# Kernel optimization log

Hardware: AMD Instinct MI355X
Metric: run time of the kernel (lower is better)

Reference implementation:

```python
import jax, jax.numpy as jnp
import numpy as np


def setup_inputs() -> dict:
    key = jax.random.key(0)
    ks = jax.random.split(key, 8)
    C = 128
    Cq = C // 8  # 16
    x = jax.random.normal(ks[0], (4, C, 64, 64), dtype=jnp.float32)
    s = 1.0 / np.sqrt(C)
    wq = jax.random.normal(ks[1], (Cq, C), dtype=jnp.float32) * s
    bq = jnp.zeros((Cq,), dtype=jnp.float32)
    wk = jax.random.normal(ks[2], (Cq, C), dtype=jnp.float32) * s
    bk = jnp.zeros((Cq,), dtype=jnp.float32)
    wv = jax.random.normal(ks[3], (C, C), dtype=jnp.float32) * s
    bv = jnp.zeros((C,), dtype=jnp.float32)
    gamma = jnp.array([0.5], dtype=jnp.float32)
    return {"x": x, "wq": wq, "bq": bq, "wk": wk, "bk": bk,
            "wv": wv, "bv": bv, "gamma": gamma}


def reference(x, wq, bq, wk, bk, wv, bv, gamma):
    B, C, W, H = x.shape
    N = W * H
    xf = x.reshape(B, C, N)  # flatten spatial; 1x1 conv == channel matmul
    q = jnp.einsum('qc,bcn->bnq', wq, xf) + bq[None, None, :]  # B,N,Cq
    k = jnp.einsum('qc,bcn->bqn', wk, xf) + bk[None, :, None]  # B,Cq,N
    v = jnp.einsum('vc,bcn->bvn', wv, xf) + bv[None, :, None]  # B,C,N
    energy = jnp.einsum('bnq,bqm->bnm', q, k)                  # B,N,N (no scaling)
    attention = jax.nn.softmax(energy, axis=-1)
    out = jnp.einsum('bvm,bnm->bvn', v, attention)             # V @ A^T
    out = out.reshape(B, C, W, H)
    return gamma[0] * out + x
```

## Files before the change

### kernel.cpp

```cpp
#include <hip/hip_runtime.h>

#define B_    4
#define C_    128
#define CQ_   16
#define N_    4096
#define KVBLK 64

typedef short          s16x8 __attribute__((ext_vector_type(8)));
typedef unsigned short u16x4 __attribute__((ext_vector_type(4)));
typedef unsigned int   u32x4 __attribute__((ext_vector_type(4)));
typedef float          f32x4 __attribute__((ext_vector_type(4)));
typedef unsigned short u16;
typedef unsigned int   u32;

__device__ __forceinline__ u16 f2bf(float f) {
    unsigned int u = __builtin_bit_cast(unsigned int, f);
    u += 0x7fffu + ((u >> 16) & 1u);
    return (u16)(u >> 16);
}
__device__ __forceinline__ float bf2f(u16 h) {
    unsigned int u = ((unsigned int)h) << 16;
    return __builtin_bit_cast(float, u);
}
__device__ __forceinline__ s16x8 ld8bf(const u16* p) {
    return *reinterpret_cast<const s16x8*>(p);
}
__device__ __forceinline__ u32 cvtpk_bf16(float lo, float hi) {
    u32 r;
    asm("v_cvt_pk_bf16_f32 %0, %1, %2" : "=v"(r) : "v"(lo), "v"(hi));
    return r;
}
__device__ __forceinline__ void gld_lds16(const u16* src, u16* lds) {
    __builtin_amdgcn_global_load_lds(
        (const __attribute__((address_space(1))) void*)src,
        (__attribute__((address_space(3))) void*)lds, 16, 0, 0);
}

__device__ __forceinline__ int invpi64(int r) {
    return (r & 0x23) | ((r & 0x10) >> 2) | ((r & 0x0C) << 1);
}

__global__ __launch_bounds__(256) void proj_all_kernel(
    const float* __restrict__ x,
    const float* __restrict__ wq, const float* __restrict__ bq,
    const float* __restrict__ wk, const float* __restrict__ bk,
    const float* __restrict__ wv, const float* __restrict__ bv,
    u16* __restrict__ Qb, u16* __restrict__ Kb, u16* __restrict__ Vb)
{
    __shared__ float smem[12800];
    const int tid = threadIdx.x;
    const int b   = blockIdx.y;
    const int nl  = tid & 63;
    const int n   = blockIdx.x * 64 + nl;
    const int ch  = tid >> 6;
    const float* xp = x + ((size_t)b * C_) * N_ + n;

    if (blockIdx.z == 0) {
        float* wqs = smem;
        float* wks = smem + 2048;
        float (*part)[4][64][17] = (float (*)[4][64][17])(smem + 4096);
        for (int i = tid; i < CQ_ * C_; i += 256) {
            const int j = i & 15, c = i >> 4;
            wqs[i] = wq[j * C_ + c];
            wks[i] = wk[j * C_ + c];
        }
        __syncthreads();

        float qa[CQ_], ka[CQ_];
#pragma unroll
        for (int j = 0; j < CQ_; ++j) { qa[j] = 0.f; ka[j] = 0.f; }
        const int c0 = ch * 32;
        for (int c = c0; c < c0 + 32; ++c) {
            const float xv = xp[(size_t)c * N_];
#pragma unroll
            for (int j = 0; j < CQ_; ++j) {
                qa[j] = fmaf(wqs[c * 16 + j], xv, qa[j]);
                ka[j] = fmaf(wks[c * 16 + j], xv, ka[j]);
            }
        }
#pragma unroll
        for (int j = 0; j < CQ_; ++j) { part[0][ch][nl][j] = qa[j]; part[1][ch][nl][j] = ka[j]; }
        __syncthreads();

        if (tid < 128) {
            const int which = tid >> 6;
            const int n2 = tid & 63;
            const float* bias = which ? bk : bq;
            const float scale = which ? 1.0f : 1.4426950408889634f;
            alignas(16) u16 row[32];
#pragma unroll
            for (int j = 0; j < CQ_; ++j) {
                float v = (part[which][0][n2][j] + part[which][1][n2][j]
                         + part[which][2][n2][j] + part[which][3][n2][j] + bias[j]) * scale;
                u16 h = f2bf(v);
                row[j]       = h;
                row[CQ_ + j] = f2bf(v - bf2f(h));
            }
            u16* dst = (which ? Kb : Qb) + ((size_t)(b * N_ + blockIdx.x * 64 + n2)) * 32;
#pragma unroll
            for (int i = 0; i < 4; ++i)
                reinterpret_cast<uint4*>(dst)[i] = reinterpret_cast<const uint4*>(row)[i];
        }
    } else {
        const int cv0 = (blockIdx.z - 1) * 32;
        float* wvs = smem;
        float (*part)[64][33] = (float (*)[64][33])(smem + 4096);
        for (int i = tid; i < 32 * C_; i += 256) {
            const int j = i & 31, c = i >> 5;
            wvs[i] = wv[(cv0 + j) * C_ + c];
        }
        __syncthreads();

        float acc[32];
#pragma unroll
        for (int j = 0; j < 32; ++j) acc[j] = 0.f;
        const int c0 = ch * 32;
        for (int c = c0; c < c0 + 32; ++c) {
            const float xv = xp[(size_t)c * N_];
#pragma unroll
            for (int j = 0; j < 32; ++j)
                acc[j] = fmaf(wvs[c * 32 + j], xv, acc[j]);
        }
#pragma unroll
        for (int j = 0; j < 32; ++j) part[ch][nl][j] = acc[j];
        __syncthreads();

        const int jq  = tid >> 6;
        const int nlp = invpi64(nl);
#pragma unroll
        for (int jj = 0; jj < 8; ++jj) {
            const int j = jq * 8 + jj;
            float v = part[0][nl][j] + part[1][nl][j] + part[2][nl][j] + part[3][nl][j]
                    + bv[cv0 + j];
            Vb[((size_t)(b * C_ + cv0 + j)) * N_ + blockIdx.x * 64 + nlp] = f2bf(v);
        }
    }
}

template<int NSPLIT>
__global__ __launch_bounds__(256, 3) void attn_split_kernel(
    const u16* __restrict__ Qb, const u16* __restrict__ Kb, const u16* __restrict__ Vb,
    u16* __restrict__ Opart, float* __restrict__ Lpart)
{
    constexpr int MPER = N_ / NSPLIT;
    constexpr int NT   = MPER / KVBLK;

    __shared__ __align__(16) u16 Kt[2][KVBLK * 32];
    __shared__ __align__(16) u16 Vt[2][C_ * KVBLK];

    const int tid  = threadIdx.x;
    const int lane = tid & 63;
    const int l16  = lane & 15;
    const int g    = lane >> 4;
    const int wave = tid >> 6;

    const int L    = blockIdx.x;
    const int grp  = (L & 7) + 8 * (L >> 8);
    const int j    = (L >> 3) & 31;
    const int b    = grp & 3;
    const int s    = grp >> 2;
    const int n0   = j * 128;
    const int ms   = s * MPER;

    const int qn = n0 + wave * 32 + l16;
    const s16x8 qf0 = ld8bf(Qb + ((size_t)(b * N_ + qn)) * 32 + 8 * g);
    const s16x8 qf1 = ld8bf(Qb + ((size_t)(b * N_ + qn + 16)) * 32 + 8 * g);

    const int kv_s   = tid >> 2;
    const int kcol_s = ((tid & 3) * 16) ^ ((kv_s & 3) << 4);
    const u16* ksrc0 = Kb + ((size_t)b * N_ + kv_s) * 32 + (kcol_s >> 1);
    const int vc_s   = tid >> 3;
    const int vcol_s = ((tid & 7) * 16) ^ ((vc_s & 7) << 4);
    const u16* vsrcB = Vb + ((size_t)(b * C_ + vc_s)) * N_ + (vcol_s >> 1);

    const int kswz  = (l16 & 3) << 4;
    const int vswz  = (l16 & 7) << 4;
    const int koff1 = l16 * 32 + (((16 * (g & 1)) ^ kswz) >> 1);
    const int koff2 = l16 * 32 + (((32 + 16 * g) ^ kswz) >> 1);
    const int voffA = l16 * 64 + (((16 * g) ^ vswz) >> 1);
    const int voffB = l16 * 64 + (((64 + 16 * g) ^ vswz) >> 1);

    const s16x8 ones = { 0x3F80, 0x3F80, 0x3F80, 0x3F80,
                         0x3F80, 0x3F80, 0x3F80, 0x3F80 };

    f32x4 acc0[8], acc1[8];
#pragma unroll
    for (int cg = 0; cg < 8; ++cg) { acc0[cg] = {}; acc1[cg] = {}; }
    f32x4 accl0 = {}, accl1 = {};

    auto packpf = [&](const float (&p)[4][4], int ss) -> s16x8 {
        u32x4 w;
        w[0] = cvtpk_bf16(p[2 * ss][0],     p[2 * ss][1]);
        w[1] = cvtpk_bf16(p[2 * ss][2],     p[2 * ss][3]);
        w[2] = cvtpk_bf16(p[2 * ss + 1][0], p[2 * ss + 1][1]);
        w[3] = cvtpk_bf16(p[2 * ss + 1][2], p[2 * ss + 1][3]);
        return __builtin_bit_cast(s16x8, w);
    };

    auto body = [&](int t, int buf) {
        if (t + 1 < NT) {
            const int mn = ms + (t + 1) * KVBLK;
            gld_lds16(ksrc0 + (size_t)mn * 32, &Kt[buf ^ 1][wave * 512]);
#pragma unroll
            for (int i = 0; i < 4; ++i)
                gld_lds16(vsrcB + (size_t)i * 32 * N_ + mn,
                          &Vt[buf ^ 1][i * 2048 + wave * 512]);
        }
        const u16* ktb = &Kt[buf][0];
        const u16* vtb = &Vt[buf][0];

        f32x4 s0[4], s1[4];
#pragma unroll
        for (int mg = 0; mg < 4; ++mg) {
            const s16x8 kf1 = ld8bf(ktb + koff1 + mg * 512);
            s16x8 kf2 = {};
            if (g < 2) kf2 = ld8bf(ktb + koff2 + mg * 512);
            f32x4 z0 = {}, z1 = {};
            z0 = __builtin_amdgcn_mfma_f32_16x16x32_bf16(kf1, qf0, z0, 0, 0, 0);
            z0 = __builtin_amdgcn_mfma_f32_16x16x32_bf16(kf2, qf0, z0, 0, 0, 0);
            z1 = __builtin_amdgcn_mfma_f32_16x16x32_bf16(kf1, qf1, z1, 0, 0, 0);
            z1 = __builtin_amdgcn_mfma_f32_16x16x32_bf16(kf2, qf1, z1, 0, 0, 0);
            s0[mg] = z0; s1[mg] = z1;
        }

        s16x8 pf0a, pf0b, pf1a, pf1b;
        {
            float p[4][4];
#pragma unroll
            for (int mg = 0; mg < 4; ++mg)
#pragma unroll
                for (int i = 0; i < 4; ++i) p[mg][i] = exp2f(s0[mg][i]);
            pf0a = packpf(p, 0); pf0b = packpf(p, 1);
        }
        {
            float p[4][4];
#pragma unroll
            for (int mg = 0; mg < 4; ++mg)
#pragma unroll
                for (int i = 0; i < 4; ++i) p[mg][i] = exp2f(s1[mg][i]);
            pf1a = packpf(p, 0); pf1b = packpf(p, 1);
        }

        accl0 = __builtin_amdgcn_mfma_f32_16x16x32_bf16(ones, pf0a, accl0, 0, 0, 0);
        accl0 = __builtin_amdgcn_mfma_f32_16x16x32_bf16(ones, pf0b, accl0, 0, 0, 0);
        accl1 = __builtin_amdgcn_mfma_f32_16x16x32_bf16(ones, pf1a, accl1, 0, 0, 0);
        accl1 = __builtin_amdgcn_mfma_f32_16x16x32_bf16(ones, pf1b, accl1, 0, 0, 0);
#pragma unroll
        for (int cg = 0; cg < 8; ++cg) {
            const s16x8 vfa = ld8bf(vtb + voffA + cg * 1024);
            acc0[cg] = __builtin_amdgcn_mfma_f32_16x16x32_bf16(vfa, pf0a, acc0[cg], 0, 0, 0);
            acc1[cg] = __builtin_amdgcn_mfma_f32_16x16x32_bf16(vfa, pf1a, acc1[cg], 0, 0, 0);
            const s16x8 vfb = ld8bf(vtb + voffB + cg * 1024);
            acc0[cg] = __builtin_amdgcn_mfma_f32_16x16x32_bf16(vfb, pf0b, acc0[cg], 0, 0, 0);
            acc1[cg] = __builtin_amdgcn_mfma_f32_16x16x32_bf16(vfb, pf1b, acc1[cg], 0, 0, 0);
        }

        asm volatile("s_waitcnt vmcnt(0)" ::: "memory");
        __syncthreads();
    };

    gld_lds16(ksrc0 + (size_t)ms * 32, &Kt[0][wave * 512]);
#pragma unroll
    for (int i = 0; i < 4; ++i)
        gld_lds16(vsrcB + (size_t)i * 32 * N_ + ms, &Vt[0][i * 2048 + wave * 512]);
    asm volatile("s_waitcnt vmcnt(0)" ::: "memory");
    __syncthreads();

    for (int tt = 0; tt < NT / 2; ++tt) {
        body(2 * tt, 0);
        body(2 * tt + 1, 1);
    }

    const size_t sb = (size_t)(s * B_ + b);
    if (lane < 16) {
        Lpart[sb * N_ + n0 + wave * 32 + l16]      = accl0[0];
        Lpart[sb * N_ + n0 + wave * 32 + 16 + l16] = accl1[0];
    }

    const int na = n0 + wave * 32 + l16;
#pragma unroll
    for (int cg = 0; cg < 8; ++cg) {
#pragma unroll
        for (int i = 0; i < 4; ++i) {
            const int c = 16 * cg + 4 * g + i;
            Opart[(sb * C_ + c) * N_ + na]      = f2bf(acc0[cg][i]);
            Opart[(sb * C_ + c) * N_ + na + 16] = f2bf(acc1[cg][i]);
        }
    }
}

template<int NSPLIT>
__global__ __launch_bounds__(256) void reduce_kernel(
    const u16* __restrict__ Opart, const float* __restrict__ Lpart,
    const float* __restrict__ x, const float* __restrict__ gamma,
    float* __restrict__ out)
{
    const int t  = blockIdx.x * 256 + threadIdx.x;
    const size_t e0 = (size_t)t * 4;
    const int n = (int)(e0 & (N_ - 1));
    const int c = (int)((e0 >> 12) & (C_ - 1));
    const int b = (int)(e0 >> 19);

    float o0 = 0.f, o1 = 0.f, o2 = 0.f, o3 = 0.f;
    f32x4 l = {};
#pragma unroll
    for (int s = 0; s < NSPLIT; ++s) {
        const size_t sb = (size_t)(s * B_ + b);
        const u16x4 ov = *reinterpret_cast<const u16x4*>(Opart + (sb * C_ + c) * N_ + n);
        const f32x4 lv = *reinterpret_cast<const f32x4*>(Lpart + sb * N_ + n);
        o0 += bf2f(ov[0]); o1 += bf2f(ov[1]); o2 += bf2f(ov[2]); o3 += bf2f(ov[3]);
        l += lv;
    }
    const float gm = gamma[0];
    const f32x4 xv = *reinterpret_cast<const f32x4*>(x + e0);
    f32x4 r;
    r[0] = gm * o0 / l[0] + xv[0];
    r[1] = gm * o1 / l[1] + xv[1];
    r[2] = gm * o2 / l[2] + xv[2];
    r[3] = gm * o3 / l[3] + xv[3];
    *reinterpret_cast<f32x4*>(out + e0) = r;
}

extern "C" void kernel_launch(void* const* d_in, const int* in_sizes, int n_in,
                              void* d_out, int out_size, void* d_ws, size_t ws_size,
                              hipStream_t stream)
{
    const float* x     = (const float*)d_in[0];
    const float* wq    = (const float*)d_in[1];
    const float* bq    = (const float*)d_in[2];
    const float* wk    = (const float*)d_in[3];
    const float* bk    = (const float*)d_in[4];
    const float* wv    = (const float*)d_in[5];
    const float* bv    = (const float*)d_in[6];
    const float* gamma = (const float*)d_in[7];
    float* out = (float*)d_out;

    u16* Qb = (u16*)d_ws;
    u16* Kb = Qb + (size_t)B_ * N_ * 32;
    u16* Vb = Kb + (size_t)B_ * N_ * 32;
    u16* Opart = Vb + (size_t)B_ * C_ * N_;
    float* Lpart = (float*)(Opart + (size_t)4 * B_ * C_ * N_);

    proj_all_kernel<<<dim3(N_ / 64, B_, 5), 256, 0, stream>>>(
        x, wq, bq, wk, bk, wv, bv, Qb, Kb, Vb);
    attn_split_kernel<4><<<dim3((N_ / 128) * B_ * 4), 256, 0, stream>>>(
        Qb, Kb, Vb, Opart, Lpart);
    reduce_kernel<4><<<(B_ * C_ * N_ / 4) / 256, 256, 0, stream>>>(
        Opart, Lpart, x, gamma, out);
}
```

Measured before the change: 71.09 us.

## Split projection work by output channel instead of input channel to drop partial-sum reduction

The projection kernel now gives each 64-thread group a slice of output channels and has it loop over all 128 input channels, so no partial sums go through shared memory and the second barrier is gone. The V projection uses 64 output channels per block, which cuts the grid z-dimension from 5 to 3 and the shared memory from 12800 to 8192 floats. Each thread now does a longer serial channel loop and every group rereads all of x, so total x traffic through the cache goes up. There are also fewer blocks in flight for the projection stage.

```diff
diff --git a/kernel.cpp b/kernel.cpp
--- a/kernel.cpp
+++ b/kernel.cpp
@@ -47,18 +47,17 @@
     const float* __restrict__ wv, const float* __restrict__ bv,
     u16* __restrict__ Qb, u16* __restrict__ Kb, u16* __restrict__ Vb)
 {
-    __shared__ float smem[12800];
+    __shared__ float smem[8192];
     const int tid = threadIdx.x;
     const int b   = blockIdx.y;
     const int nl  = tid & 63;
     const int n   = blockIdx.x * 64 + nl;
-    const int ch  = tid >> 6;
+    const int grp = tid >> 6;
     const float* xp = x + ((size_t)b * C_) * N_ + n;
 
     if (blockIdx.z == 0) {
         float* wqs = smem;
         float* wks = smem + 2048;
-        float (*part)[4][64][17] = (float (*)[4][64][17])(smem + 4096);
         for (int i = tid; i < CQ_ * C_; i += 256) {
             const int j = i & 15, c = i >> 4;
             wqs[i] = wq[j * C_ + c];
@@ -66,73 +65,58 @@
         }
         __syncthreads();
 
-        float qa[CQ_], ka[CQ_];
-#pragma unroll
-        for (int j = 0; j < CQ_; ++j) { qa[j] = 0.f; ka[j] = 0.f; }
-        const int c0 = ch * 32;
-        for (int c = c0; c < c0 + 32; ++c) {
+        const bool isk = (grp >= 2);
+        const int  j0  = (grp & 1) * 8;
+        const float* ws = isk ? wks : wqs;
+
+        float acc[8];
+#pragma unroll
+        for (int j = 0; j < 8; ++j) acc[j] = 0.f;
+        for (int c = 0; c < C_; ++c) {
             const float xv = xp[(size_t)c * N_];
 #pragma unroll
-            for (int j = 0; j < CQ_; ++j) {
-                qa[j] = fmaf(wqs[c * 16 + j], xv, qa[j]);
-                ka[j] = fmaf(wks[c * 16 + j], xv, ka[j]);
-            }
-        }
-#pragma unroll
-        for (int j = 0; j < CQ_; ++j) { part[0][ch][nl][j] = qa[j]; part[1][ch][nl][j] = ka[j]; }
+            for (int j = 0; j < 8; ++j)
+                acc[j] = fmaf(ws[c * 16 + j0 + j], xv, acc[j]);
+        }
+
+        const float* bias = isk ? bk : bq;
+        const float scale = isk ? 1.0f : 1.4426950408889634f;
+        alignas(16) u16 hi[8], lo[8];
+#pragma unroll
+        for (int j = 0; j < 8; ++j) {
+            const float v = (acc[j] + bias[j0 + j]) * scale;
+            const u16 h = f2bf(v);
+            hi[j] = h;
+            lo[j] = f2bf(v - bf2f(h));
+        }
+        u16* dst = (isk ? Kb : Qb) + ((size_t)(b * N_ + n)) * 32 + j0;
+        *reinterpret_cast<uint4*>(dst)      = *reinterpret_cast<const uint4*>(hi);
+        *reinterpret_cast<uint4*>(dst + 16) = *reinterpret_cast<const uint4*>(lo);
+    } else {
+        const int cv0 = (blockIdx.z - 1) * 64;
+        float* wvs = smem;
+        for (int i = tid; i < 64 * C_; i += 256) {
+            const int j = i & 63, c = i >> 6;
+            wvs[i] = wv[(cv0 + j) * C_ + c];
+        }
         __syncthreads();
 
-        if (tid < 128) {
-            const int which = tid >> 6;
-            const int n2 = tid & 63;
-            const float* bias = which ? bk : bq;
-            const float scale = which ? 1.0f : 1.4426950408889634f;
-            alignas(16) u16 row[32];
-#pragma unroll
-            for (int j = 0; j < CQ_; ++j) {
-                float v = (part[which][0][n2][j] + part[which][1][n2][j]
-                         + part[which][2][n2][j] + part[which][3][n2][j] + bias[j]) * scale;
-                u16 h = f2bf(v);
-                row[j]       = h;
-                row[CQ_ + j] = f2bf(v - bf2f(h));
-            }
-            u16* dst = (which ? Kb : Qb) + ((size_t)(b * N_ + blockIdx.x * 64 + n2)) * 32;
-#pragma unroll
-            for (int i = 0; i < 4; ++i)
-                reinterpret_cast<uint4*>(dst)[i] = reinterpret_cast<const uint4*>(row)[i];
-        }
-    } else {
-        const int cv0 = (blockIdx.z - 1) * 32;
-        float* wvs = smem;
-        float (*part)[64][33] = (float (*)[64][33])(smem + 4096);
-        for (int i = tid; i < 32 * C_; i += 256) {
-            const int j = i & 31, c = i >> 5;
-            wvs[i] = wv[(cv0 + j) * C_ + c];
-        }
-        __syncthreads();
-
-        float acc[32];
-#pragma unroll
-        for (int j = 0; j < 32; ++j) acc[j] = 0.f;
-        const int c0 = ch * 32;
-        for (int c = c0; c < c0 + 32; ++c) {
+        const int j0 = grp * 16;
+        float acc[16];
+#pragma unroll
+        for (int j = 0; j < 16; ++j) acc[j] = 0.f;
+        for (int c = 0; c < C_; ++c) {
             const float xv = xp[(size_t)c * N_];
 #pragma unroll
-            for (int j = 0; j < 32; ++j)
-                acc[j] = fmaf(wvs[c * 32 + j], xv, acc[j]);
-        }
-#pragma unroll
-        for (int j = 0; j < 32; ++j) part[ch][nl][j] = acc[j];
-        __syncthreads();
-
-        const int jq  = tid >> 6;
+            for (int j = 0; j < 16; ++j)
+                acc[j] = fmaf(wvs[c * 64 + j0 + j], xv, acc[j]);
+        }
+
         const int nlp = invpi64(nl);
 #pragma unroll
-        for (int jj = 0; jj < 8; ++jj) {
-            const int j = jq * 8 + jj;
-            float v = part[0][nl][j] + part[1][nl][j] + part[2][nl][j] + part[3][nl][j]
-                    + bv[cv0 + j];
-            Vb[((size_t)(b * C_ + cv0 + j)) * N_ + blockIdx.x * 64 + nlp] = f2bf(v);
+        for (int j = 0; j < 16; ++j) {
+            const float v = acc[j] + bv[cv0 + j0 + j];
+            Vb[((size_t)(b * C_ + cv0 + j0 + j)) * N_ + blockIdx.x * 64 + nlp] = f2bf(v);
         }
     }
 }
@@ -341,7 +325,7 @@
     u16* Opart = Vb + (size_t)B_ * C_ * N_;
     float* Lpart = (float*)(Opart + (size_t)4 * B_ * C_ * N_);
 
-    proj_all_kernel<<<dim3(N_ / 64, B_, 5), 256, 0, stream>>>(
+    proj_all_kernel<<<dim3(N_ / 64, B_, 3), 256, 0, stream>>>(
         x, wq, bq, wk, bk, wv, bv, Qb, Kb, Vb);
     attn_split_kernel<4><<<dim3((N_ / 128) * B_ * 4), 256, 0, stream>>>(
         Qb, Kb, Vb, Opart, Lpart);
```

Result: slower. 72.67 us (+2.2%).
